# Optimization experiments

Measured on AMD Instinct MI355X. Metric: run time of the kernel, lower is better.

## Reference

```python
import jax, jax.numpy as jnp
import numpy as np

N_EDGES = 50000
KMAX = 16
NUM_SPH = 16
EMB = 64
INTERM = 64
UNITS_OUT = 128
K_FILL = 8  # occupied neighbor slots per edge -> nTriplets = N_EDGES * K_FILL


def setup_inputs() -> dict:
    key = jax.random.key(0)
    k1, k2, k3, k4 = jax.random.split(key, 4)
    rbf_W1 = jax.random.normal(k1, (N_EDGES, INTERM, NUM_SPH), dtype=jnp.float32)
    sph = jax.random.normal(k2, (N_EDGES, NUM_SPH, KMAX), dtype=jnp.float32)
    m = jax.random.normal(k3, (N_EDGES * K_FILL, EMB), dtype=jnp.float32)
    weight = jax.random.normal(k4, (EMB, INTERM, UNITS_OUT), dtype=jnp.float32) * (1.0 / np.sqrt(EMB * INTERM))
    # Unique (edge, slot) pairs: each edge occupies slots 0..K_FILL-1 of the padded matrix.
    id_reduce = jnp.repeat(jnp.arange(N_EDGES, dtype=jnp.int64), K_FILL)
    Kidx = jnp.tile(jnp.arange(K_FILL, dtype=jnp.int64), N_EDGES)
    return {"rbf_W1": rbf_W1, "sph": sph, "m": m, "weight": weight,
            "id_reduce": id_reduce, "Kidx": Kidx}


def reference(rbf_W1, sph, m, weight, id_reduce, Kidx):
    nEdges = rbf_W1.shape[0]
    Kmax = sph.shape[2]
    emb_size = m.shape[1]
    # Scatter triplet embeddings into the zero-padded dense neighbor matrix.
    m2 = jnp.zeros((nEdges, Kmax, emb_size), dtype=m.dtype)
    m2 = m2.at[id_reduce, Kidx].set(m)  # (nEdges, Kmax, emb)
    # sum over neighbors weighted by spherical basis: (nEdges, num_sph, emb)
    sum_k = jnp.matmul(sph, m2)
    # down-projected radial basis contraction: (nEdges, interm, emb)
    rbf_W1_sum_k = jnp.matmul(rbf_W1, sum_k)
    # bilinear layer + sum over emb axis, fused into one contraction:
    # original: permute->(emb,nEdges,interm) @ weight(emb,interm,units) then sum over emb
    m_ca = jnp.einsum("nie,eiu->nu", rbf_W1_sum_k, weight)  # (nEdges, units_out)
    return m_ca
```

## Files before the change

kernel.cpp:

```cpp
#include <hip/hip_runtime.h>

#define NE     50000
#define KMAX   16
#define NSPH   16
#define EMB    64
#define INTERM 64
#define UOUT   128

#define EPB    32
#define LPW    4

typedef __attribute__((ext_vector_type(4))) float v4f;
typedef __attribute__((ext_vector_type(4))) short s4;
typedef __attribute__((ext_vector_type(8))) short s8;

__device__ inline unsigned short f2b(float x){
  union { float f; unsigned int u; } v; v.f = x;
  unsigned int r = v.u + 0x7FFFu + ((v.u >> 16) & 1u);
  return (unsigned short)(r >> 16);
}

__device__ inline s4 cvt4(v4f v){
  s4 r;
  r.x = (short)f2b(v.x); r.y = (short)f2b(v.y);
  r.z = (short)f2b(v.z); r.w = (short)f2b(v.w);
  return r;
}

__device__ inline void lds_barrier(){
  asm volatile("s_waitcnt lgkmcnt(0)" ::: "memory");
  __builtin_amdgcn_s_barrier();
}

__global__ void scatter_map_kernel(const int* __restrict__ idr, const int* __restrict__ kidx,
                                   int* __restrict__ map, int n){
  int t = blockIdx.x * 256 + threadIdx.x;
  if (t < n) map[idr[t] * KMAX + kidx[t]] = t;
}

__global__ void pack_w_kernel(const float* __restrict__ wgt, unsigned short* __restrict__ wb){
  int o = blockIdx.x * 256 + threadIdx.x;
  int j  = o & 7;
  int rest = o >> 3;
  int u  = rest & 127;
  int kb = rest >> 7;
  int k  = kb * 8 + j;
  int ic = k >> 10, rem = k & 1023, hf = rem >> 9, r2 = rem & 511, il = r2 >> 5, ch = r2 & 31;
  int i = ic * 16 + il, c = hf * 32 + ch;
  wb[o] = f2b(wgt[c * (INTERM * UOUT) + i * UOUT + u]);
}

__global__ __launch_bounds__(512, 4)
void fused_kernel(const float* __restrict__ rbf,
                  const float* __restrict__ sph,
                  const float* __restrict__ m,
                  const unsigned short* __restrict__ wb,
                  const int* __restrict__ map,
                  float* __restrict__ out)
{
  __shared__ __align__(16) unsigned short Tlds[EPB * 1024];
  const int tid = threadIdx.x;
  const int l = tid & 63;
  const int w = tid >> 6;
  const int q = l >> 4;
  const int h = l & 15;
  const int ebase = blockIdx.x * EPB;

  s4 Sfrag[LPW][4];
#pragma unroll
  for (int le = 0; le < LPW; ++le){
    int e = ebase + w * LPW + le; if (e >= NE) e = NE - 1;
    s4 a = cvt4(*reinterpret_cast<const v4f*>(sph + e * 256 + h * 16 + q * 4));
    int t0 = map[e * 16 + q * 4 + 0];
    int t1 = map[e * 16 + q * 4 + 1];
    int t2 = map[e * 16 + q * 4 + 2];
    int t3 = map[e * 16 + q * 4 + 3];
#pragma unroll
    for (int ct = 0; ct < 4; ++ct){
      int c = ct * 16 + h;
      s4 b;
      b.x = (t0 >= 0) ? (short)f2b(m[t0 * 64 + c]) : (short)0;
      b.y = (t1 >= 0) ? (short)f2b(m[t1 * 64 + c]) : (short)0;
      b.z = (t2 >= 0) ? (short)f2b(m[t2 * 64 + c]) : (short)0;
      b.w = (t3 >= 0) ? (short)f2b(m[t3 * 64 + c]) : (short)0;
      v4f acc = {0.f, 0.f, 0.f, 0.f};
      acc = __builtin_amdgcn_mfma_f32_16x16x16bf16_1k(a, b, acc, 0, 0, 0);
      Sfrag[le][ct] = cvt4(acc);
    }
  }

  v4f Oacc[2];
#pragma unroll
  for (int mt = 0; mt < 2; ++mt) Oacc[mt] = (v4f){0.f, 0.f, 0.f, 0.f};

  v4f Araw[LPW];
#pragma unroll
  for (int le = 0; le < LPW; ++le){
    int e = ebase + w * LPW + le; if (e >= NE) e = NE - 1;
    Araw[le] = *reinterpret_cast<const v4f*>(rbf + (size_t)e * 1024 + h * 16 + q * 4);
  }

#pragma unroll 1
  for (int ic = 0; ic < 4; ++ic){
#pragma unroll
    for (int le = 0; le < LPW; ++le){
      s4 Acvt = cvt4(Araw[le]);
      int row = w * LPW + le;
#pragma unroll
      for (int ct = 0; ct < 4; ++ct){
        v4f acc = {0.f, 0.f, 0.f, 0.f};
        acc = __builtin_amdgcn_mfma_f32_16x16x16bf16_1k(Sfrag[le][ct], Acvt, acc, 0, 0, 0);
        s4 tv = cvt4(acc);
        int b  = (ct >> 1) * 64 + h * 4 + (ct & 1) * 2 + (q >> 1);
        int bs = b ^ (row & 7) ^ (((b >> 4) & 3) << 1);
        *reinterpret_cast<s4*>(&Tlds[row * 1024 + bs * 8 + (q & 1) * 4]) = tv;
      }
      int icn = (ic < 3) ? ic + 1 : 3;
      int e = ebase + w * LPW + le; if (e >= NE) e = NE - 1;
      Araw[le] = *reinterpret_cast<const v4f*>(rbf + (size_t)e * 1024 + (icn * 16 + h) * 16 + q * 4);
    }
    lds_barrier();

    const unsigned short* wptr = wb + (size_t)ic * 131072 + (size_t)q * 1024 + (size_t)(w * 16 + h) * 8;
    s8 bf[4], nf[4];
#pragma unroll
    for (int j = 0; j < 4; ++j)
      bf[j] = *reinterpret_cast<const s8*>(wptr + j * 4096);
#pragma unroll 1
    for (int kc = 0; kc < 8; ++kc){
      const unsigned short* np = wptr + (size_t)((kc < 7) ? kc + 1 : 7) * 16384;
#pragma unroll
      for (int j = 0; j < 4; ++j)
        nf[j] = *reinterpret_cast<const s8*>(np + j * 4096);
#pragma unroll
      for (int j = 0; j < 4; ++j){
        int ks = kc * 4 + j;
        int bb = ks * 4 + q;
        int bsw = bb ^ (h & 7) ^ (((bb >> 4) & 3) << 1);
        s8 afr0 = *reinterpret_cast<const s8*>(&Tlds[h * 1024 + bsw * 8]);
        s8 afr1 = *reinterpret_cast<const s8*>(&Tlds[(16 + h) * 1024 + bsw * 8]);
        Oacc[0] = __builtin_amdgcn_mfma_f32_16x16x32_bf16(afr0, bf[j], Oacc[0], 0, 0, 0);
        Oacc[1] = __builtin_amdgcn_mfma_f32_16x16x32_bf16(afr1, bf[j], Oacc[1], 0, 0, 0);
      }
#pragma unroll
      for (int j = 0; j < 4; ++j) bf[j] = nf[j];
    }
    lds_barrier();
  }

#pragma unroll
  for (int mt = 0; mt < 2; ++mt){
#pragma unroll
    for (int r = 0; r < 4; ++r){
      int e = ebase + mt * 16 + q * 4 + r;
      if (e < NE) out[e * 128 + w * 16 + h] = Oacc[mt][r];
    }
  }
}

extern "C" void kernel_launch(void* const* d_in, const int* in_sizes, int n_in,
                              void* d_out, int out_size, void* d_ws, size_t ws_size,
                              hipStream_t stream) {
  const float* rbf = (const float*)d_in[0];
  const float* sph = (const float*)d_in[1];
  const float* m   = (const float*)d_in[2];
  const float* wgt = (const float*)d_in[3];
  const int* idr  = (const int*)d_in[4];
  const int* kidx = (const int*)d_in[5];
  float* out = (float*)d_out;

  const int nTrip = in_sizes[4];
  int*            map = (int*)d_ws;
  unsigned short* wb  = (unsigned short*)((char*)d_ws + (size_t)NE * 16 * 4);

  hipMemsetAsync(map, 0xFF, (size_t)NE * 16 * 4, stream);
  scatter_map_kernel<<<dim3((nTrip + 255) / 256), dim3(256), 0, stream>>>(idr, kidx, map, nTrip);
  pack_w_kernel<<<dim3((EMB * INTERM * UOUT) / 256), dim3(256), 0, stream>>>(wgt, wb);
  fused_kernel<<<dim3((NE + EPB - 1) / EPB), dim3(512), 0, stream>>>(rbf, sph, m, wb, map, out);
}
```

Before: 555.4 us.

## Split second GEMM over K across wave halves with LDS reduction

The work split of the final bilinear GEMM is reorganized. Each wave now covers 32 output units and half of the K dimension, instead of 16 units and the full K. This lets each A fragment read from LDS be reused across two B fragments, halving LDS reads per MFMA, and replaces the chunked double-buffer weight prefetch with a rolling per-slot prefetch. The two K-halves are then summed through an LDS reduction plus an extra barrier before the store. The m loads are also rewritten to gather floats first and convert them as one vector.

After: 514.4 us. 1.08x faster.

```diff
diff --git a/kernel.cpp b/kernel.cpp
--- a/kernel.cpp
+++ b/kernel.cpp
@@ -65,6 +65,8 @@
   const int q = l >> 4;
   const int h = l & 15;
   const int ebase = blockIdx.x * EPB;
+  const int kq = w >> 2;
+  const int uh = w & 3;
 
   s4 Sfrag[LPW][4];
 #pragma unroll
@@ -78,20 +80,23 @@
 #pragma unroll
     for (int ct = 0; ct < 4; ++ct){
       int c = ct * 16 + h;
-      s4 b;
-      b.x = (t0 >= 0) ? (short)f2b(m[t0 * 64 + c]) : (short)0;
-      b.y = (t1 >= 0) ? (short)f2b(m[t1 * 64 + c]) : (short)0;
-      b.z = (t2 >= 0) ? (short)f2b(m[t2 * 64 + c]) : (short)0;
-      b.w = (t3 >= 0) ? (short)f2b(m[t3 * 64 + c]) : (short)0;
+      float fx = 0.f, fy = 0.f, fz = 0.f, fw = 0.f;
+      if (t0 >= 0) fx = m[t0 * 64 + c];
+      if (t1 >= 0) fy = m[t1 * 64 + c];
+      if (t2 >= 0) fz = m[t2 * 64 + c];
+      if (t3 >= 0) fw = m[t3 * 64 + c];
+      s4 b = cvt4((v4f){fx, fy, fz, fw});
       v4f acc = {0.f, 0.f, 0.f, 0.f};
       acc = __builtin_amdgcn_mfma_f32_16x16x16bf16_1k(a, b, acc, 0, 0, 0);
       Sfrag[le][ct] = cvt4(acc);
     }
   }
 
-  v4f Oacc[2];
-#pragma unroll
-  for (int mt = 0; mt < 2; ++mt) Oacc[mt] = (v4f){0.f, 0.f, 0.f, 0.f};
+  v4f Oacc[2][2];
+#pragma unroll
+  for (int mt = 0; mt < 2; ++mt)
+#pragma unroll
+    for (int ub = 0; ub < 2; ++ub) Oacc[mt][ub] = (v4f){0.f, 0.f, 0.f, 0.f};
 
   v4f Araw[LPW];
 #pragma unroll
@@ -121,40 +126,59 @@
     }
     lds_barrier();
 
-    const unsigned short* wptr = wb + (size_t)ic * 131072 + (size_t)q * 1024 + (size_t)(w * 16 + h) * 8;
-    s8 bf[4], nf[4];
-#pragma unroll
-    for (int j = 0; j < 4; ++j)
-      bf[j] = *reinterpret_cast<const s8*>(wptr + j * 4096);
+    const unsigned short* wp = wb + ((size_t)(ic * 128 + kq * 64 + q) * 128 + uh * 32 + h) * 8;
+    s8 F[4][2];
+#pragma unroll
+    for (int ss = 0; ss < 4; ++ss){
+      F[ss][0] = *reinterpret_cast<const s8*>(wp + ss * 4096);
+      F[ss][1] = *reinterpret_cast<const s8*>(wp + ss * 4096 + 128);
+    }
 #pragma unroll 1
-    for (int kc = 0; kc < 8; ++kc){
-      const unsigned short* np = wptr + (size_t)((kc < 7) ? kc + 1 : 7) * 16384;
-#pragma unroll
-      for (int j = 0; j < 4; ++j)
-        nf[j] = *reinterpret_cast<const s8*>(np + j * 4096);
-#pragma unroll
-      for (int j = 0; j < 4; ++j){
-        int ks = kc * 4 + j;
-        int bb = ks * 4 + q;
+    for (int sc = 0; sc < 4; ++sc){
+#pragma unroll
+      for (int ss = 0; ss < 4; ++ss){
+        int s = sc * 4 + ss;
+        int bb = kq * 64 + s * 4 + q;
         int bsw = bb ^ (h & 7) ^ (((bb >> 4) & 3) << 1);
         s8 afr0 = *reinterpret_cast<const s8*>(&Tlds[h * 1024 + bsw * 8]);
         s8 afr1 = *reinterpret_cast<const s8*>(&Tlds[(16 + h) * 1024 + bsw * 8]);
-        Oacc[0] = __builtin_amdgcn_mfma_f32_16x16x32_bf16(afr0, bf[j], Oacc[0], 0, 0, 0);
-        Oacc[1] = __builtin_amdgcn_mfma_f32_16x16x32_bf16(afr1, bf[j], Oacc[1], 0, 0, 0);
+        Oacc[0][0] = __builtin_amdgcn_mfma_f32_16x16x32_bf16(afr0, F[ss][0], Oacc[0][0], 0, 0, 0);
+        Oacc[1][0] = __builtin_amdgcn_mfma_f32_16x16x32_bf16(afr1, F[ss][0], Oacc[1][0], 0, 0, 0);
+        Oacc[0][1] = __builtin_amdgcn_mfma_f32_16x16x32_bf16(afr0, F[ss][1], Oacc[0][1], 0, 0, 0);
+        Oacc[1][1] = __builtin_amdgcn_mfma_f32_16x16x32_bf16(afr1, F[ss][1], Oacc[1][1], 0, 0, 0);
+        int sn = (s + 4 < 16) ? s + 4 : s;
+        F[ss][0] = *reinterpret_cast<const s8*>(wp + sn * 4096);
+        F[ss][1] = *reinterpret_cast<const s8*>(wp + sn * 4096 + 128);
       }
-#pragma unroll
-      for (int j = 0; j < 4; ++j) bf[j] = nf[j];
     }
     lds_barrier();
   }
 
-#pragma unroll
-  for (int mt = 0; mt < 2; ++mt){
-#pragma unroll
-    for (int r = 0; r < 4; ++r){
-      int e = ebase + mt * 16 + q * 4 + r;
-      if (e < NE) out[e * 128 + w * 16 + h] = Oacc[mt][r];
-    }
+  float* red = reinterpret_cast<float*>(Tlds);
+  if (kq == 1){
+#pragma unroll
+    for (int mt = 0; mt < 2; ++mt)
+#pragma unroll
+      for (int ub = 0; ub < 2; ++ub)
+#pragma unroll
+        for (int r = 0; r < 4; ++r){
+          int row = mt * 16 + q * 4 + r;
+          red[uh * 1024 + row * 32 + ub * 16 + h] = Oacc[mt][ub][r];
+        }
+  }
+  lds_barrier();
+  if (kq == 0){
+#pragma unroll
+    for (int mt = 0; mt < 2; ++mt)
+#pragma unroll
+      for (int ub = 0; ub < 2; ++ub)
+#pragma unroll
+        for (int r = 0; r < 4; ++r){
+          int row = mt * 16 + q * 4 + r;
+          float v = Oacc[mt][ub][r] + red[uh * 1024 + row * 32 + ub * 16 + h];
+          int e = ebase + row;
+          if (e < NE) out[e * 128 + uh * 32 + ub * 16 + h] = v;
+        }
   }
 }
 
```
